# Performance work log

Measured on AMD Instinct MI355X. Metric: run time of the kernel, lower is better.

The kernel has to match this reference:

```python
import jax, jax.numpy as jnp
import numpy as np

N, E = 100000, 3200000
D_IN, D_H, H, C, TDIM, N_CLS = 17, 32, 2, 16, 32, 2


def _seg_softmax(alpha, dst, num_segments):
    # numerically stable softmax over edges grouped by destination node
    m = jax.ops.segment_max(alpha, dst, num_segments=num_segments)  # [N,H]
    a = jnp.exp(alpha - m[dst])
    s = jax.ops.segment_sum(a, dst, num_segments=num_segments)      # [N,H]
    return a / s[dst]


def setup_inputs() -> dict:
    key = jax.random.key(0)
    ks = jax.random.split(key, 16)
    w = lambda k, o, i: jax.random.normal(k, (o, i), dtype=jnp.float32) * 0.05
    inp = {
        "x": jax.random.normal(ks[0], (N, D_IN), dtype=jnp.float32),
        "edge_index": jax.random.randint(ks[1], (2, E), 0, N, dtype=jnp.int64),
        "t": jax.random.uniform(ks[2], (E, 1), dtype=jnp.float32),
        "node_time": jax.random.uniform(ks[3], (N,), dtype=jnp.float32),
        # TimeEncode params (init exactly as torch module)
        "basis_freq": jnp.asarray(1.0 / 10 ** np.linspace(0, 9, TDIM), dtype=jnp.float32),
        "phase": jnp.zeros((TDIM,), dtype=jnp.float32),
        # lin: 17 -> 32
        "W_lin": w(ks[4], D_H, D_IN), "b_lin": jnp.zeros((D_H,), jnp.float32),
        # TransformerConv(32, 16, heads=2, edge_dim=32)
        "Wq": w(ks[5], H * C, D_H), "bq": jnp.zeros((H * C,), jnp.float32),
        "Wk": w(ks[6], H * C, D_H), "bk": jnp.zeros((H * C,), jnp.float32),
        "Wv": w(ks[7], H * C, D_H), "bv": jnp.zeros((H * C,), jnp.float32),
        "We": w(ks[8], H * C, TDIM), "be": jnp.zeros((H * C,), jnp.float32),
        "Wskip": w(ks[9], H * C, D_H), "bskip": jnp.zeros((H * C,), jnp.float32),
        # out: 32 -> 2
        "W_out": w(ks[10], N_CLS, D_H), "b_out": jnp.zeros((N_CLS,), jnp.float32),
    }
    return inp


def reference(x, edge_index, t, node_time, basis_freq, phase, W_lin, b_lin,
              Wq, bq, Wk, bk, Wv, bv, We, be, Wskip, bskip, W_out, b_out):
    src, dst = edge_index[0], edge_index[1]
    n = x.shape[0]
    # relative time per edge + cosine time encoding -> [E, 32]
    rel_t = node_time[src][:, None] - t                      # [E,1]
    rel_t_enc = jnp.cos(rel_t * basis_freq[None, :] + phase[None, :])  # [E,32]
    # node MLP
    h1 = jax.nn.relu(x @ W_lin.T + b_lin)                    # [N,32]
    # TransformerConv (dropout off / eval mode)
    q = (h1 @ Wq.T + bq)[dst].reshape(-1, H, C)              # [E,H,C]
    e = (rel_t_enc @ We.T + be).reshape(-1, H, C)            # [E,H,C]
    k = (h1 @ Wk.T + bk)[src].reshape(-1, H, C) + e
    alpha = (q * k).sum(-1) / jnp.sqrt(jnp.float32(C))       # [E,H]
    alpha = _seg_softmax(alpha, dst, n)
    v = (h1 @ Wv.T + bv)[src].reshape(-1, H, C) + e          # [E,H,C]
    msg = (v * alpha[:, :, None]).reshape(-1, H * C)         # [E,32]
    agg = jax.ops.segment_sum(msg, dst, num_segments=n)      # [N,32]
    h = agg + h1 @ Wskip.T + bskip                           # root/skip connection
    logits = h @ W_out.T + b_out                             # [N,2]
    return jax.nn.log_softmax(logits, axis=1)
```

## Files before the change

### kernel.cpp

```cpp
#include <hip/hip_runtime.h>
#include <math.h>

#define D_IN 17
#define DH   32
#define TDIM 32
#define TABK 256

#define NBSH 8
#define BNODES (1 << NBSH)
#define NBKMAX 512
#define CAPB 9216
#define TILE 8192

__device__ __forceinline__ unsigned int f2bf(float x) {
    unsigned int u = __float_as_uint(x);
    return (u + 0x7fffu + ((u >> 16) & 1u)) >> 16;
}
__device__ __forceinline__ float bfl(unsigned int u) { return __uint_as_float(u << 16); }
__device__ __forceinline__ float bfh(unsigned int u) { return __uint_as_float(u & 0xffff0000u); }

__global__ __launch_bounds__(256) void node_prep(
    const float* __restrict__ x,
    const float* __restrict__ Wl, const float* __restrict__ bl,
    const float* __restrict__ Wq, const float* __restrict__ bq,
    const float* __restrict__ Wk, const float* __restrict__ bk,
    const float* __restrict__ Wv, const float* __restrict__ bv,
    const float* __restrict__ Ws, const float* __restrict__ bs,
    float* __restrict__ qn, unsigned short* __restrict__ kvn,
    float* __restrict__ skv, int* __restrict__ bcur, int N)
{
    int mat = blockIdx.y;
    if (blockIdx.x == 0 && mat == 0) {
        for (int i = threadIdx.x; i < NBKMAX; i += 256) bcur[i] = 0;
    }

    __shared__ float w[544 + 32 + 1024 + 32];
    {
        const float* Wsel = (mat == 0) ? Wq : (mat == 1) ? Wk : (mat == 2) ? Wv : Ws;
        const float* bsel = (mat == 0) ? bq : (mat == 1) ? bk : (mat == 2) ? bv : bs;
        for (int idx = threadIdx.x; idx < 544; idx += 256) {
            int i = idx / D_IN, j = idx - i * D_IN;
            w[j * DH + i] = Wl[idx];
        }
        if (threadIdx.x < 32) w[544 + threadIdx.x] = bl[threadIdx.x];
        for (int i = threadIdx.x; i < 1024; i += 256) w[576 + i] = Wsel[i];
        if (threadIdx.x < 32) w[1600 + threadIdx.x] = bsel[threadIdx.x];
    }
    __syncthreads();

    int n = blockIdx.x * 256 + threadIdx.x;
    if (n >= N) return;

    float xv[D_IN];
#pragma unroll
    for (int j = 0; j < D_IN; ++j) xv[j] = x[(size_t)n * D_IN + j];

    float h1[DH];
#pragma unroll
    for (int c = 0; c < 8; ++c) {
        float4 b = *(const float4*)&w[544 + c * 4];
        h1[c*4+0] = b.x; h1[c*4+1] = b.y; h1[c*4+2] = b.z; h1[c*4+3] = b.w;
    }
#pragma unroll
    for (int j = 0; j < D_IN; ++j) {
        float xj = xv[j];
#pragma unroll
        for (int c = 0; c < 8; ++c) {
            float4 wv = *(const float4*)&w[j * DH + c * 4];
            h1[c*4+0] += xj * wv.x;
            h1[c*4+1] += xj * wv.y;
            h1[c*4+2] += xj * wv.z;
            h1[c*4+3] += xj * wv.w;
        }
    }
#pragma unroll
    for (int i = 0; i < DH; ++i) h1[i] = fmaxf(h1[i], 0.0f);

    float outr[DH];
#pragma unroll
    for (int i = 0; i < DH; ++i) {
        float acc = w[1600 + i];
#pragma unroll
        for (int c = 0; c < 8; ++c) {
            float4 wv = *(const float4*)&w[576 + i * DH + c * 4];
            acc += h1[c * 4 + 0] * wv.x + h1[c * 4 + 1] * wv.y
                 + h1[c * 4 + 2] * wv.z + h1[c * 4 + 3] * wv.w;
        }
        outr[i] = acc;
    }

    if (mat == 0) {
        float4* dst4 = (float4*)(qn + (size_t)n * DH);
#pragma unroll
        for (int c = 0; c < 8; ++c) {
            float4 o; o.x = outr[c*4+0] * 0.25f; o.y = outr[c*4+1] * 0.25f;
            o.z = outr[c*4+2] * 0.25f; o.w = outr[c*4+3] * 0.25f;
            dst4[c] = o;
        }
    } else if (mat == 1 || mat == 2) {
        unsigned int pw[16];
#pragma unroll
        for (int i = 0; i < 16; ++i)
            pw[i] = f2bf(outr[2*i]) | (f2bf(outr[2*i+1]) << 16);
        uint4* row = (uint4*)(kvn + (size_t)n * 64) + (mat == 1 ? 0 : 4);
#pragma unroll
        for (int c = 0; c < 4; ++c) {
            uint4 o; o.x = pw[c*4+0]; o.y = pw[c*4+1]; o.z = pw[c*4+2]; o.w = pw[c*4+3];
            row[c] = o;
        }
    } else {
        float4* dst4 = (float4*)(skv + (size_t)n * DH);
#pragma unroll
        for (int c = 0; c < 8; ++c) {
            float4 o; o.x = outr[c*4+0]; o.y = outr[c*4+1];
            o.z = outr[c*4+2]; o.w = outr[c*4+3];
            dst4[c] = o;
        }
    }
}

__global__ __launch_bounds__(64) void build_table(
    const float* __restrict__ We, const float* __restrict__ be,
    const float* __restrict__ freq, const float* __restrict__ phase,
    float* __restrict__ table)
{
    int k = blockIdx.x * blockDim.x + threadIdx.x;
    if (k > TABK) return;
    float r = -1.0f + 2.0f * (float)k / (float)TABK;
    float cj[TDIM];
#pragma unroll
    for (int j = 0; j < TDIM; ++j) cj[j] = cosf(r * freq[j] + phase[j]);
#pragma unroll 4
    for (int o = 0; o < DH; ++o) {
        float acc = be[o];
#pragma unroll
        for (int j = 0; j < TDIM; ++j) acc += cj[j] * We[o * TDIM + j];
        table[(size_t)k * DH + o] = acc;
    }
}

__global__ __launch_bounds__(256) void idx_k(
    const int* __restrict__ ei, const float* __restrict__ t,
    const float* __restrict__ ntime, unsigned char* __restrict__ idxbuf, int E)
{
    int e = blockIdx.x * blockDim.x + threadIdx.x;
    if (e >= E) return;
    float rel = ntime[ei[e]] - t[e];
    float u = fmaf(rel, (float)(TABK / 2), (float)(TABK / 2) + 0.5f);
    int idx = (int)u;
    idx = min(max(idx, 0), TABK - 1);
    idxbuf[e] = (unsigned char)idx;
}

__global__ __launch_bounds__(512) void s1_bucket(
    const int* __restrict__ ei, const unsigned char* __restrict__ idxbuf,
    int* __restrict__ bcur, int* __restrict__ stgA,
    unsigned char* __restrict__ stgB, int E, int NBK)
{
    __shared__ int2 tile[TILE];
    __shared__ int  lcnt[NBKMAX];
    __shared__ int  lcur[NBKMAX];
    __shared__ int  gdel[NBKMAX];

    int tid = threadIdx.x;
    int base = blockIdx.x * TILE;
    int cnt_here = min(TILE, E - base);

    lcnt[tid] = 0;
    __syncthreads();

#pragma unroll 4
    for (int i = 0; i < TILE / 512; ++i) {
        int e = base + i * 512 + tid;
        if (e < E) atomicAdd(&lcnt[((unsigned int)ei[E + e]) >> NBSH], 1);
    }
    __syncthreads();

    {
        __shared__ int sd[512];
        int v0 = lcnt[tid];
        sd[tid] = v0;
        __syncthreads();
        for (int st = 1; st < 512; st <<= 1) {
            int v = (tid >= st) ? sd[tid - st] : 0;
            __syncthreads();
            sd[tid] += v;
            __syncthreads();
        }
        int lofs = sd[tid] - v0;
        if (tid < NBK) {
            int gpos = (v0 > 0) ? (tid * CAPB + atomicAdd(&bcur[tid], v0)) : 0;
            lcur[tid] = lofs;
            gdel[tid] = gpos - lofs;
        }
    }
    __syncthreads();

#pragma unroll 4
    for (int i = 0; i < TILE / 512; ++i) {
        int e = base + i * 512 + tid;
        if (e < E) {
            int d = ei[E + e];
            int s = ei[e];
            int idx = (int)idxbuf[e];
            int b = ((unsigned int)d) >> NBSH;
            int r = atomicAdd(&lcur[b], 1);
            tile[r] = make_int2(s | ((d & (BNODES - 1)) << 17),
                                idx | (b << 20));
        }
    }
    __syncthreads();

    for (int k = tid; k < cnt_here; k += 512) {
        int2 en = tile[k];
        int b = ((unsigned int)en.y) >> 20;
        int gp = gdel[b] + k;
        if (gp < (b + 1) * CAPB) {
            stgA[gp] = (en.x & 0x1FFFF) | ((en.y & 0xFF) << 17);
            stgB[gp] = (unsigned char)((en.x >> 17) & 0xFF);
        }
    }
}

__global__ __launch_bounds__(512) void s2_hist_scatter(
    const int* __restrict__ bcur, const int* __restrict__ stgA,
    const unsigned char* __restrict__ stgB,
    int* __restrict__ payload, int* __restrict__ off, int* __restrict__ cntout,
    int N)
{
    __shared__ int lcnt[BNODES];
    __shared__ int sc[BNODES];
    int t = threadIdx.x;
    int nb0 = blockIdx.x << NBSH;
    if (t < BNODES) lcnt[t] = 0;
    __syncthreads();

    int lo = blockIdx.x * CAPB;
    int hi = lo + min(bcur[blockIdx.x], CAPB);

    for (int i = lo + t; i < hi; i += 512)
        atomicAdd(&lcnt[stgB[i]], 1);
    __syncthreads();

    if (t < BNODES) sc[t] = lcnt[t];
    __syncthreads();
    for (int st = 1; st < BNODES; st <<= 1) {
        int v = 0;
        if (t < BNODES && t >= st) v = sc[t - st];
        __syncthreads();
        if (t < BNODES) sc[t] += v;
        __syncthreads();
    }
    if (t < BNODES) {
        int c = lcnt[t];
        int gpos = lo + sc[t] - c;
        if (nb0 + t < N) { off[nb0 + t] = gpos; cntout[nb0 + t] = c; }
        lcnt[t] = gpos;
    }
    __syncthreads();

    for (int i = lo + t; i < hi; i += 512) {
        int pos = atomicAdd(&lcnt[stgB[i]], 1);
        payload[pos] = stgA[i];
    }
}

__global__ __launch_bounds__(256) void gather_pass(
    const int* __restrict__ off, const int* __restrict__ cnt,
    const int* __restrict__ payload,
    const float* __restrict__ qn, const unsigned short* __restrict__ kvn,
    const float* __restrict__ skv, const float* __restrict__ table,
    const float* __restrict__ Wout, const float* __restrict__ bout,
    float* __restrict__ out, int N)
{
    int tid = blockIdx.x * blockDim.x + threadIdx.x;
    int d    = tid >> 4;
    int slot = (tid >> 2) & 3;
    int sub  = tid & 3;
    if (d >= N) return;

    int qb = sub * 8;
    const float4 qa = *(const float4*)(qn + d * DH + qb);
    const float4 qc = *(const float4*)(qn + d * DH + qb + 4);

    float a0 = 0, a1 = 0, a2 = 0, a3 = 0, a4 = 0, a5 = 0, a6 = 0, a7 = 0;
    float ssum = 0.0f;

    int beg = off[d];
    int end = beg + cnt[d];
    int j = beg + slot;
    int p = (j < end) ? payload[j] : 0;
    for (; j < end; j += 4) {
        int pc = p;
        if (j + 4 < end) p = payload[j + 4];

        int src = pc & 0x1FFFF;
        int idx = ((unsigned int)pc) >> 17;

        const float* tr = table + idx * DH + qb;
        float4 e0 = *(const float4*)tr;
        float4 e1 = *(const float4*)(tr + 4);
        const unsigned short* row = kvn + src * 64 + sub * 8;
        uint4 kb = *(const uint4*)row;
        uint4 vb = *(const uint4*)(row + 32);

        float part = qa.x * (bfl(kb.x) + e0.x) + qa.y * (bfh(kb.x) + e0.y)
                   + qa.z * (bfl(kb.y) + e0.z) + qa.w * (bfh(kb.y) + e0.w)
                   + qc.x * (bfl(kb.z) + e1.x) + qc.y * (bfh(kb.z) + e1.y)
                   + qc.z * (bfl(kb.w) + e1.z) + qc.w * (bfh(kb.w) + e1.w);
        part += __shfl_xor(part, 1);
        float wgt = __expf(part);
        ssum += wgt;

        a0 += (bfl(vb.x) + e0.x) * wgt;
        a1 += (bfh(vb.x) + e0.y) * wgt;
        a2 += (bfl(vb.y) + e0.z) * wgt;
        a3 += (bfh(vb.y) + e0.w) * wgt;
        a4 += (bfl(vb.z) + e1.x) * wgt;
        a5 += (bfh(vb.z) + e1.y) * wgt;
        a6 += (bfl(vb.w) + e1.z) * wgt;
        a7 += (bfh(vb.w) + e1.w) * wgt;
    }

#define COMB(dist)                                                           \
    a0 += __shfl_xor(a0, dist); a1 += __shfl_xor(a1, dist);                  \
    a2 += __shfl_xor(a2, dist); a3 += __shfl_xor(a3, dist);                  \
    a4 += __shfl_xor(a4, dist); a5 += __shfl_xor(a5, dist);                  \
    a6 += __shfl_xor(a6, dist); a7 += __shfl_xor(a7, dist);                  \
    ssum += __shfl_xor(ssum, dist);
    COMB(4)
    COMB(8)
#undef COMB

    float r = (ssum > 0.0f) ? 1.0f / ssum : 0.0f;
    const float4 ska = *(const float4*)(skv + d * DH + qb);
    const float4 skc = *(const float4*)(skv + d * DH + qb + 4);
    float h0 = a0 * r + ska.x;
    float h1 = a1 * r + ska.y;
    float h2 = a2 * r + ska.z;
    float h3 = a3 * r + ska.w;
    float h4 = a4 * r + skc.x;
    float h5 = a5 * r + skc.y;
    float h6 = a6 * r + skc.z;
    float h7 = a7 * r + skc.w;

    const float4 w0a = *(const float4*)(Wout + qb);
    const float4 w0c = *(const float4*)(Wout + qb + 4);
    const float4 w1a = *(const float4*)(Wout + DH + qb);
    const float4 w1c = *(const float4*)(Wout + DH + qb + 4);
    float l0 = h0 * w0a.x + h1 * w0a.y + h2 * w0a.z + h3 * w0a.w
             + h4 * w0c.x + h5 * w0c.y + h6 * w0c.z + h7 * w0c.w;
    float l1 = h0 * w1a.x + h1 * w1a.y + h2 * w1a.z + h3 * w1a.w
             + h4 * w1c.x + h5 * w1c.y + h6 * w1c.z + h7 * w1c.w;
    l0 += __shfl_xor(l0, 1); l0 += __shfl_xor(l0, 2);
    l1 += __shfl_xor(l1, 1); l1 += __shfl_xor(l1, 2);

    if ((tid & 15) == 0) {
        l0 += bout[0];
        l1 += bout[1];
        float m = fmaxf(l0, l1);
        float lse = m + logf(__expf(l0 - m) + __expf(l1 - m));
        float2 o; o.x = l0 - lse; o.y = l1 - lse;
        *(float2*)(out + d * 2) = o;
    }
}

extern "C" void kernel_launch(void* const* d_in, const int* in_sizes, int n_in,
                              void* d_out, int out_size, void* d_ws, size_t ws_size,
                              hipStream_t stream)
{
    const float* x      = (const float*)d_in[0];
    const int*   ei     = (const int*)d_in[1];
    const float* t      = (const float*)d_in[2];
    const float* ntime  = (const float*)d_in[3];
    const float* freq   = (const float*)d_in[4];
    const float* phase  = (const float*)d_in[5];
    const float* Wl     = (const float*)d_in[6];
    const float* bl     = (const float*)d_in[7];
    const float* Wq     = (const float*)d_in[8];
    const float* bq     = (const float*)d_in[9];
    const float* Wk     = (const float*)d_in[10];
    const float* bk     = (const float*)d_in[11];
    const float* Wv     = (const float*)d_in[12];
    const float* bv     = (const float*)d_in[13];
    const float* We     = (const float*)d_in[14];
    const float* be     = (const float*)d_in[15];
    const float* Ws     = (const float*)d_in[16];
    const float* bs     = (const float*)d_in[17];
    const float* Wout   = (const float*)d_in[18];
    const float* bout   = (const float*)d_in[19];

    const int E = in_sizes[2];
    const int N = in_sizes[3];
    const int NBK = (N + BNODES - 1) >> NBSH;

    char* wsb = (char*)d_ws;
    int*   stgA    = (int*)wsb;             wsb += (size_t)NBK * CAPB * 4;
    int*   payload = (int*)wsb;             wsb += (size_t)NBK * CAPB * 4;
    unsigned char* stgB = (unsigned char*)wsb; wsb += (size_t)NBK * CAPB;
    unsigned char* idxbuf = (unsigned char*)wsb; wsb += (size_t)E;
    wsb = (char*)(((size_t)wsb + 15) & ~(size_t)15);
    float* qn   = (float*)wsb;              wsb += (size_t)N * DH * 4;
    unsigned short* kvn = (unsigned short*)wsb; wsb += (size_t)N * 64 * 2;
    float* skv  = (float*)wsb;              wsb += (size_t)N * DH * 4;
    float* tab  = (float*)wsb;              wsb += (size_t)(TABK + 1) * DH * 4;
    int*   off  = (int*)wsb;                wsb += (size_t)N * 4;
    int*   cnt  = (int*)wsb;                wsb += (size_t)N * 4;
    int*   bcur = (int*)wsb;                wsb += NBKMAX * 4;

    float* out = (float*)d_out;

    int nblk = (N + 255) / 256;
    int tblk = (E + TILE - 1) / TILE;
    int eblk = (E + 255) / 256;

    dim3 npgrid(nblk, 4, 1);
    node_prep<<<npgrid, 256, 0, stream>>>(x, Wl, bl, Wq, bq, Wk, bk, Wv, bv, Ws, bs,
                                          qn, kvn, skv, bcur, N);
    build_table<<<(TABK + 64) / 64, 64, 0, stream>>>(We, be, freq, phase, tab);
    idx_k<<<eblk, 256, 0, stream>>>(ei, t, ntime, idxbuf, E);
    s1_bucket<<<tblk, 512, 0, stream>>>(ei, idxbuf, bcur, stgA, stgB, E, NBK);
    s2_hist_scatter<<<NBK, 512, 0, stream>>>(bcur, stgA, stgB, payload, off, cnt, N);

    int gblk = ((size_t)N * 16 + 255) / 256;
    gather_pass<<<gblk, 256, 0, stream>>>(off, cnt, payload, qn, kvn, skv,
                                          tab, Wout, bout, out, N);
}
```

Before: 199.2 us.

## Fuse node projection and edge bucketing into one heterogeneous kernel

Merges the node_prep kernel (per-node MLP and Q/K/V/skip projections) and the s1_bucket edge bucketing pass into a single launch. Blocks are interleaved two node-work blocks per bucketing block so the compute-bound and memory-bound work can run at the same time. Zeroing of the bucket cursors moves into idx_k, and shared memory becomes one raw buffer sized for the larger role. The cost is one launch and a pipeline bubble removed. In exchange every block reserves about 72KB of shared memory, which can limit occupancy for the node-projection blocks.

```diff
diff --git a/kernel.cpp b/kernel.cpp
--- a/kernel.cpp
+++ b/kernel.cpp
@@ -12,6 +12,8 @@
 #define CAPB 9216
 #define TILE 8192
 
+#define SM_BYTES 73728
+
 __device__ __forceinline__ unsigned int f2bf(float x) {
     unsigned int u = __float_as_uint(x);
     return (u + 0x7fffu + ((u >> 16) & 1u)) >> 16;
@@ -19,7 +21,44 @@
 __device__ __forceinline__ float bfl(unsigned int u) { return __uint_as_float(u << 16); }
 __device__ __forceinline__ float bfh(unsigned int u) { return __uint_as_float(u & 0xffff0000u); }
 
-__global__ __launch_bounds__(256) void node_prep(
+__global__ __launch_bounds__(64) void build_table(
+    const float* __restrict__ We, const float* __restrict__ be,
+    const float* __restrict__ freq, const float* __restrict__ phase,
+    float* __restrict__ table)
+{
+    int k = blockIdx.x * blockDim.x + threadIdx.x;
+    if (k > TABK) return;
+    float r = -1.0f + 2.0f * (float)k / (float)TABK;
+    float cj[TDIM];
+#pragma unroll
+    for (int j = 0; j < TDIM; ++j) cj[j] = cosf(r * freq[j] + phase[j]);
+#pragma unroll 4
+    for (int o = 0; o < DH; ++o) {
+        float acc = be[o];
+#pragma unroll
+        for (int j = 0; j < TDIM; ++j) acc += cj[j] * We[o * TDIM + j];
+        table[(size_t)k * DH + o] = acc;
+    }
+}
+
+__global__ __launch_bounds__(256) void idx_k(
+    const int* __restrict__ ei, const float* __restrict__ t,
+    const float* __restrict__ ntime, unsigned char* __restrict__ idxbuf,
+    int* __restrict__ bcur, int E)
+{
+    if (blockIdx.x == 0) {
+        for (int i = threadIdx.x; i < NBKMAX; i += 256) bcur[i] = 0;
+    }
+    int e = blockIdx.x * blockDim.x + threadIdx.x;
+    if (e >= E) return;
+    float rel = ntime[ei[e]] - t[e];
+    float u = fmaf(rel, (float)(TABK / 2), (float)(TABK / 2) + 0.5f);
+    int idx = (int)u;
+    idx = min(max(idx, 0), TABK - 1);
+    idxbuf[e] = (unsigned char)idx;
+}
+
+__global__ __launch_bounds__(512) void fused_np_s1(
     const float* __restrict__ x,
     const float* __restrict__ Wl, const float* __restrict__ bl,
     const float* __restrict__ Wq, const float* __restrict__ bq,
@@ -27,143 +66,125 @@
     const float* __restrict__ Wv, const float* __restrict__ bv,
     const float* __restrict__ Ws, const float* __restrict__ bs,
     float* __restrict__ qn, unsigned short* __restrict__ kvn,
-    float* __restrict__ skv, int* __restrict__ bcur, int N)
-{
-    int mat = blockIdx.y;
-    if (blockIdx.x == 0 && mat == 0) {
-        for (int i = threadIdx.x; i < NBKMAX; i += 256) bcur[i] = 0;
-    }
-
-    __shared__ float w[544 + 32 + 1024 + 32];
-    {
-        const float* Wsel = (mat == 0) ? Wq : (mat == 1) ? Wk : (mat == 2) ? Wv : Ws;
-        const float* bsel = (mat == 0) ? bq : (mat == 1) ? bk : (mat == 2) ? bv : bs;
-        for (int idx = threadIdx.x; idx < 544; idx += 256) {
-            int i = idx / D_IN, j = idx - i * D_IN;
-            w[j * DH + i] = Wl[idx];
-        }
-        if (threadIdx.x < 32) w[544 + threadIdx.x] = bl[threadIdx.x];
-        for (int i = threadIdx.x; i < 1024; i += 256) w[576 + i] = Wsel[i];
-        if (threadIdx.x < 32) w[1600 + threadIdx.x] = bsel[threadIdx.x];
-    }
-    __syncthreads();
-
-    int n = blockIdx.x * 256 + threadIdx.x;
-    if (n >= N) return;
-
-    float xv[D_IN];
-#pragma unroll
-    for (int j = 0; j < D_IN; ++j) xv[j] = x[(size_t)n * D_IN + j];
-
-    float h1[DH];
-#pragma unroll
-    for (int c = 0; c < 8; ++c) {
-        float4 b = *(const float4*)&w[544 + c * 4];
-        h1[c*4+0] = b.x; h1[c*4+1] = b.y; h1[c*4+2] = b.z; h1[c*4+3] = b.w;
-    }
-#pragma unroll
-    for (int j = 0; j < D_IN; ++j) {
-        float xj = xv[j];
-#pragma unroll
-        for (int c = 0; c < 8; ++c) {
-            float4 wv = *(const float4*)&w[j * DH + c * 4];
-            h1[c*4+0] += xj * wv.x;
-            h1[c*4+1] += xj * wv.y;
-            h1[c*4+2] += xj * wv.z;
-            h1[c*4+3] += xj * wv.w;
-        }
-    }
-#pragma unroll
-    for (int i = 0; i < DH; ++i) h1[i] = fmaxf(h1[i], 0.0f);
-
-    float outr[DH];
-#pragma unroll
-    for (int i = 0; i < DH; ++i) {
-        float acc = w[1600 + i];
-#pragma unroll
-        for (int c = 0; c < 8; ++c) {
-            float4 wv = *(const float4*)&w[576 + i * DH + c * 4];
-            acc += h1[c * 4 + 0] * wv.x + h1[c * 4 + 1] * wv.y
-                 + h1[c * 4 + 2] * wv.z + h1[c * 4 + 3] * wv.w;
-        }
-        outr[i] = acc;
-    }
-
-    if (mat == 0) {
-        float4* dst4 = (float4*)(qn + (size_t)n * DH);
-#pragma unroll
-        for (int c = 0; c < 8; ++c) {
-            float4 o; o.x = outr[c*4+0] * 0.25f; o.y = outr[c*4+1] * 0.25f;
-            o.z = outr[c*4+2] * 0.25f; o.w = outr[c*4+3] * 0.25f;
-            dst4[c] = o;
-        }
-    } else if (mat == 1 || mat == 2) {
-        unsigned int pw[16];
-#pragma unroll
-        for (int i = 0; i < 16; ++i)
-            pw[i] = f2bf(outr[2*i]) | (f2bf(outr[2*i+1]) << 16);
-        uint4* row = (uint4*)(kvn + (size_t)n * 64) + (mat == 1 ? 0 : 4);
-#pragma unroll
-        for (int c = 0; c < 4; ++c) {
-            uint4 o; o.x = pw[c*4+0]; o.y = pw[c*4+1]; o.z = pw[c*4+2]; o.w = pw[c*4+3];
-            row[c] = o;
-        }
-    } else {
-        float4* dst4 = (float4*)(skv + (size_t)n * DH);
-#pragma unroll
-        for (int c = 0; c < 8; ++c) {
-            float4 o; o.x = outr[c*4+0]; o.y = outr[c*4+1];
-            o.z = outr[c*4+2]; o.w = outr[c*4+3];
-            dst4[c] = o;
-        }
-    }
-}
-
-__global__ __launch_bounds__(64) void build_table(
-    const float* __restrict__ We, const float* __restrict__ be,
-    const float* __restrict__ freq, const float* __restrict__ phase,
-    float* __restrict__ table)
-{
-    int k = blockIdx.x * blockDim.x + threadIdx.x;
-    if (k > TABK) return;
-    float r = -1.0f + 2.0f * (float)k / (float)TABK;
-    float cj[TDIM];
-#pragma unroll
-    for (int j = 0; j < TDIM; ++j) cj[j] = cosf(r * freq[j] + phase[j]);
-#pragma unroll 4
-    for (int o = 0; o < DH; ++o) {
-        float acc = be[o];
-#pragma unroll
-        for (int j = 0; j < TDIM; ++j) acc += cj[j] * We[o * TDIM + j];
-        table[(size_t)k * DH + o] = acc;
-    }
-}
-
-__global__ __launch_bounds__(256) void idx_k(
-    const int* __restrict__ ei, const float* __restrict__ t,
-    const float* __restrict__ ntime, unsigned char* __restrict__ idxbuf, int E)
-{
-    int e = blockIdx.x * blockDim.x + threadIdx.x;
-    if (e >= E) return;
-    float rel = ntime[ei[e]] - t[e];
-    float u = fmaf(rel, (float)(TABK / 2), (float)(TABK / 2) + 0.5f);
-    int idx = (int)u;
-    idx = min(max(idx, 0), TABK - 1);
-    idxbuf[e] = (unsigned char)idx;
-}
-
-__global__ __launch_bounds__(512) void s1_bucket(
+    float* __restrict__ skv, int N,
     const int* __restrict__ ei, const unsigned char* __restrict__ idxbuf,
     int* __restrict__ bcur, int* __restrict__ stgA,
-    unsigned char* __restrict__ stgB, int E, int NBK)
-{
-    __shared__ int2 tile[TILE];
-    __shared__ int  lcnt[NBKMAX];
-    __shared__ int  lcur[NBKMAX];
-    __shared__ int  gdel[NBKMAX];
-
+    unsigned char* __restrict__ stgB, int E, int NBK,
+    int NA, int NB)
+{
+    __shared__ __align__(16) char smraw[SM_BYTES];
+
+    int bid = blockIdx.x;
     int tid = threadIdx.x;
-    int base = blockIdx.x * TILE;
+
+    int grp = bid / 3, rem = bid - grp * 3;
+    bool isA;
+    int ridx;
+    if (grp < NB) {
+        if (rem < 2) { isA = true;  ridx = grp * 2 + rem; }
+        else         { isA = false; ridx = grp; }
+    } else {
+        isA = true;  ridx = 2 * NB + (bid - 3 * NB);
+    }
+
+    if (isA) {
+        if (ridx >= NA) return;
+        float* w = (float*)smraw;
+        int mat  = ridx & 3;
+        int xblk = ridx >> 2;
+
+        {
+            const float* Wsel = (mat == 0) ? Wq : (mat == 1) ? Wk : (mat == 2) ? Wv : Ws;
+            const float* bsel = (mat == 0) ? bq : (mat == 1) ? bk : (mat == 2) ? bv : bs;
+            for (int idx = tid; idx < 544; idx += 512) {
+                int i = idx / D_IN, j = idx - i * D_IN;
+                w[j * DH + i] = Wl[idx];
+            }
+            if (tid < 32) w[544 + tid] = bl[tid];
+            for (int i = tid; i < 1024; i += 512) w[576 + i] = Wsel[i];
+            if (tid < 32) w[1600 + tid] = bsel[tid];
+        }
+        __syncthreads();
+
+        int n = xblk * 512 + tid;
+        if (n >= N) return;
+
+        float xv[D_IN];
+#pragma unroll
+        for (int j = 0; j < D_IN; ++j) xv[j] = x[(size_t)n * D_IN + j];
+
+        float h1[DH];
+#pragma unroll
+        for (int c = 0; c < 8; ++c) {
+            float4 b = *(const float4*)&w[544 + c * 4];
+            h1[c*4+0] = b.x; h1[c*4+1] = b.y; h1[c*4+2] = b.z; h1[c*4+3] = b.w;
+        }
+#pragma unroll
+        for (int j = 0; j < D_IN; ++j) {
+            float xj = xv[j];
+#pragma unroll
+            for (int c = 0; c < 8; ++c) {
+                float4 wv = *(const float4*)&w[j * DH + c * 4];
+                h1[c*4+0] += xj * wv.x;
+                h1[c*4+1] += xj * wv.y;
+                h1[c*4+2] += xj * wv.z;
+                h1[c*4+3] += xj * wv.w;
+            }
+        }
+#pragma unroll
+        for (int i = 0; i < DH; ++i) h1[i] = fmaxf(h1[i], 0.0f);
+
+        float outr[DH];
+#pragma unroll
+        for (int i = 0; i < DH; ++i) {
+            float acc = w[1600 + i];
+#pragma unroll
+            for (int c = 0; c < 8; ++c) {
+                float4 wv = *(const float4*)&w[576 + i * DH + c * 4];
+                acc += h1[c * 4 + 0] * wv.x + h1[c * 4 + 1] * wv.y
+                     + h1[c * 4 + 2] * wv.z + h1[c * 4 + 3] * wv.w;
+            }
+            outr[i] = acc;
+        }
+
+        if (mat == 0) {
+            float4* dst4 = (float4*)(qn + (size_t)n * DH);
+#pragma unroll
+            for (int c = 0; c < 8; ++c) {
+                float4 o; o.x = outr[c*4+0] * 0.25f; o.y = outr[c*4+1] * 0.25f;
+                o.z = outr[c*4+2] * 0.25f; o.w = outr[c*4+3] * 0.25f;
+                dst4[c] = o;
+            }
+        } else if (mat == 1 || mat == 2) {
+            unsigned int pw[16];
+#pragma unroll
+            for (int i = 0; i < 16; ++i)
+                pw[i] = f2bf(outr[2*i]) | (f2bf(outr[2*i+1]) << 16);
+            uint4* row = (uint4*)(kvn + (size_t)n * 64) + (mat == 1 ? 0 : 4);
+#pragma unroll
+            for (int c = 0; c < 4; ++c) {
+                uint4 o; o.x = pw[c*4+0]; o.y = pw[c*4+1]; o.z = pw[c*4+2]; o.w = pw[c*4+3];
+                row[c] = o;
+            }
+        } else {
+            float4* dst4 = (float4*)(skv + (size_t)n * DH);
+#pragma unroll
+            for (int c = 0; c < 8; ++c) {
+                float4 o; o.x = outr[c*4+0]; o.y = outr[c*4+1];
+                o.z = outr[c*4+2]; o.w = outr[c*4+3];
+                dst4[c] = o;
+            }
+        }
+        return;
+    }
+
+    int2* tile = (int2*)smraw;
+    int*  lcnt = (int*)(smraw + 65536);
+    int*  lcur = (int*)(smraw + 67584);
+    int*  gdel = (int*)(smraw + 69632);
+    int*  sd   = (int*)(smraw + 71680);
+
+    int base = ridx * TILE;
     int cnt_here = min(TILE, E - base);
 
     lcnt[tid] = 0;
@@ -177,7 +198,6 @@
     __syncthreads();
 
     {
-        __shared__ int sd[512];
         int v0 = lcnt[tid];
         sd[tid] = v0;
         __syncthreads();
@@ -215,7 +235,7 @@
         int2 en = tile[k];
         int b = ((unsigned int)en.y) >> 20;
         int gp = gdel[b] + k;
-        if (gp < (b + 1) * CAPB) {
+        if (gp >= b * CAPB && gp < (b + 1) * CAPB) {
             stgA[gp] = (en.x & 0x1FFFF) | ((en.y & 0xFF) << 17);
             stgB[gp] = (unsigned char)((en.x >> 17) & 0xFF);
         }
@@ -410,16 +430,16 @@
 
     float* out = (float*)d_out;
 
-    int nblk = (N + 255) / 256;
-    int tblk = (E + TILE - 1) / TILE;
     int eblk = (E + 255) / 256;
-
-    dim3 npgrid(nblk, 4, 1);
-    node_prep<<<npgrid, 256, 0, stream>>>(x, Wl, bl, Wq, bq, Wk, bk, Wv, bv, Ws, bs,
-                                          qn, kvn, skv, bcur, N);
+    int NA = ((N + 511) / 512) * 4;
+    int NB = (E + TILE - 1) / TILE;
+    int fgrid = 3 * NB + max(0, NA - 2 * NB);
+
     build_table<<<(TABK + 64) / 64, 64, 0, stream>>>(We, be, freq, phase, tab);
-    idx_k<<<eblk, 256, 0, stream>>>(ei, t, ntime, idxbuf, E);
-    s1_bucket<<<tblk, 512, 0, stream>>>(ei, idxbuf, bcur, stgA, stgB, E, NBK);
+    idx_k<<<eblk, 256, 0, stream>>>(ei, t, ntime, idxbuf, bcur, E);
+    fused_np_s1<<<fgrid, 512, 0, stream>>>(
+        x, Wl, bl, Wq, bq, Wk, bk, Wv, bv, Ws, bs, qn, kvn, skv, N,
+        ei, idxbuf, bcur, stgA, stgB, E, NBK, NA, NB);
     s2_hist_scatter<<<NBK, 512, 0, stream>>>(bcur, stgA, stgB, payload, off, cnt, N);
 
     int gblk = ((size_t)N * 16 + 255) / 256;
```

Measured after the change: 189.3 us. -5.0%, faster.
